# Kernel tuning notes

Measured on AMD Instinct MI355X. Metric: run time of the kernel, lower is better.

Reference implementation:

```python
import jax, jax.numpy as jnp
import numpy as np


def setup_inputs() -> dict:
    key = jax.random.key(0)
    k1, k2, k3, k4 = jax.random.split(key, 4)
    B, S, K, N = 2, 1024, 4096, 4096
    x = jax.random.normal(k1, (B, S, K), dtype=jnp.float32)
    # int8 weights in [-128, 127]
    weight = jax.random.randint(k2, (N, K), -128, 128, dtype=jnp.int8)
    # per-output-channel dequant scales (small positive values)
    scales = jax.random.uniform(k3, (N,), dtype=jnp.float32, minval=0.005, maxval=0.02)
    bias = jax.random.normal(k4, (N,), dtype=jnp.float32) * 0.1
    return {"x": x, "weight": weight, "scales": scales, "bias": bias}


def reference(x, weight, scales, bias):
    # F.linear(x, weight.to(x.dtype)): [B,S,K] @ [N,K]^T -> [B,S,N]
    w = weight.astype(x.dtype)
    y = jnp.einsum('bsk,nk->bsn', x, w)
    # per-output-channel scale + bias epilogue
    return y * scales + bias
```

## Files before the change

kernel.cpp:

```cpp
#include <hip/hip_runtime.h>
#include <hip/hip_bf16.h>
#include <stdint.h>

#define M_DIM 2048
#define N_DIM 4096
#define K_DIM 4096

#define BM 128
#define BN 128
#define BK 128

#define ATILE (BM * BK)
#define BTILE (BN * BK)
#define NT (K_DIM / BK)

typedef __attribute__((ext_vector_type(4))) int   int4v;
typedef __attribute__((ext_vector_type(4))) float f32x4;

__device__ __forceinline__ void load_lds16(const void* g, void* l) {
    __builtin_amdgcn_global_load_lds(
        (const __attribute__((address_space(1))) void*)g,
        (__attribute__((address_space(3))) void*)l,
        16, 0, 0);
}

__global__ __launch_bounds__(256) void quant_x(const float* __restrict__ x,
                                               int8_t* __restrict__ Aq,
                                               float* __restrict__ sx) {
    const int row = blockIdx.x;
    const int tid = threadIdx.x;
    const float4* xr = (const float4*)(x + (size_t)row * K_DIM);

    float4 v[4];
    float mx = 0.f;
#pragma unroll
    for (int p = 0; p < 4; p++) {
        v[p] = xr[p * 256 + tid];
        mx = fmaxf(mx, fmaxf(fmaxf(fabsf(v[p].x), fabsf(v[p].y)),
                             fmaxf(fabsf(v[p].z), fabsf(v[p].w))));
    }
#pragma unroll
    for (int off = 32; off >= 1; off >>= 1)
        mx = fmaxf(mx, __shfl_xor(mx, off, 64));

    __shared__ float wmax[4];
    __shared__ float smax;
    if ((tid & 63) == 0) wmax[tid >> 6] = mx;
    __syncthreads();
    if (tid == 0) {
        float m = fmaxf(fmaxf(wmax[0], wmax[1]), fmaxf(wmax[2], wmax[3]));
        m = fmaxf(m, 1e-20f);
        smax = m;
        sx[row] = m * (1.0f / 127.0f);
    }
    __syncthreads();
    const float inv = 127.0f / smax;

    int* out = (int*)Aq + (size_t)row * (K_DIM / 4);
#pragma unroll
    for (int p = 0; p < 4; p++) {
        int q0 = (int)__builtin_rintf(v[p].x * inv);
        int q1 = (int)__builtin_rintf(v[p].y * inv);
        int q2 = (int)__builtin_rintf(v[p].z * inv);
        int q3 = (int)__builtin_rintf(v[p].w * inv);
        q0 = max(-127, min(127, q0)); q1 = max(-127, min(127, q1));
        q2 = max(-127, min(127, q2)); q3 = max(-127, min(127, q3));
        out[p * 256 + tid] = (q0 & 255) | ((q1 & 255) << 8) |
                             ((q2 & 255) << 16) | ((q3 & 255) << 24);
    }
}

__global__ __launch_bounds__(256) void cvt_w8(const int* __restrict__ w,
                                              int8_t* __restrict__ Bq) {
    size_t i = ((size_t)blockIdx.x * 256 + threadIdx.x) * 16;
    int4 a0 = *(const int4*)(w + i);
    int4 a1 = *(const int4*)(w + i + 4);
    int4 a2 = *(const int4*)(w + i + 8);
    int4 a3 = *(const int4*)(w + i + 12);
    uint4 t;
    t.x = (a0.x & 255) | ((a0.y & 255) << 8) | ((a0.z & 255) << 16) | ((a0.w & 255) << 24);
    t.y = (a1.x & 255) | ((a1.y & 255) << 8) | ((a1.z & 255) << 16) | ((a1.w & 255) << 24);
    t.z = (a2.x & 255) | ((a2.y & 255) << 8) | ((a2.z & 255) << 16) | ((a2.w & 255) << 24);
    t.w = (a3.x & 255) | ((a3.y & 255) << 8) | ((a3.z & 255) << 16) | ((a3.w & 255) << 24);
    *(uint4*)(Bq + i) = t;
}


__global__ __launch_bounds__(512, 4) void gemm_bt_i8(
    const int8_t* __restrict__ A,
    const int8_t* __restrict__ B,
    const float*  __restrict__ sx,
    const float*  __restrict__ scales,
    const float*  __restrict__ bias,
    float* __restrict__ C)
{
    __shared__ __align__(16) int8_t As[2 * ATILE];
    __shared__ __align__(16) int8_t Bs[2 * BTILE];

    const int tid  = threadIdx.x;

    const int bid   = blockIdx.x;
    const int xcd   = bid & 7;
    const int local = bid >> 3;
    const int bm    = (xcd >> 2) * 8 + (local >> 3);
    const int bn    = (xcd & 3) * 8 + (local & 7);

    const int lane = tid & 63;
    const int wave = tid >> 6;
    const int spat = wave & 3;
    const int ks   = wave >> 2;
    const int wm   = (spat >> 1) * 64;
    const int wn   = (spat & 1) * 64;
    const int l16  = lane & 15;
    const int quad = lane >> 4;
    const int swz  = l16 & 7;
    const int cp   = (ks * 4 + quad) ^ swz;

    const int srow = tid >> 3;
    const int cgl  = (tid & 7) ^ (srow & 7);

    const int8_t* ga0 = A + (size_t)(bm * BM + srow)      * K_DIM + cgl * 16;
    const int8_t* ga1 = A + (size_t)(bm * BM + 64 + srow) * K_DIM + cgl * 16;
    const int8_t* gb0 = B + (size_t)(bn * BN + srow)      * K_DIM + cgl * 16;
    const int8_t* gb1 = B + (size_t)(bn * BN + 64 + srow) * K_DIM + cgl * 16;
    const int la0 = tid * 16;
    const int la1 = 8192 + tid * 16;

    load_lds16(ga0, As + la0);
    load_lds16(ga1, As + la1);
    load_lds16(gb0, Bs + la0);
    load_lds16(gb1, Bs + la1);

    int4v acc[4][4] = {};

    int cur = 0;
    for (int k0 = 0; k0 < K_DIM; k0 += BK, cur ^= 1) {
        __syncthreads();

        const int kn = k0 + BK;
        if (kn < K_DIM) {
            const int nb = (cur ^ 1);
            load_lds16(ga0 + kn, As + nb * ATILE + la0);
            load_lds16(ga1 + kn, As + nb * ATILE + la1);
            load_lds16(gb0 + kn, Bs + nb * BTILE + la0);
            load_lds16(gb1 + kn, Bs + nb * BTILE + la1);
        }

        const int8_t* Ab = As + cur * ATILE;
        const int8_t* Bb = Bs + cur * BTILE;

        int4v af[4];
#pragma unroll
        for (int i = 0; i < 4; i++)
            af[i] = *(const int4v*)(Ab + (wm + i * 16 + l16) * BK + cp * 16);
#pragma unroll
        for (int j = 0; j < 4; j++) {
            int4v bf = *(const int4v*)(Bb + (wn + j * 16 + l16) * BK + cp * 16);
#pragma unroll
            for (int i = 0; i < 4; i++)
                acc[i][j] = __builtin_amdgcn_mfma_i32_16x16x64_i8(
                    af[i], bf, acc[i][j], 0, 0, 0);
        }
    }

    __syncthreads();

    int8_t* rbase = (spat < 2 ? As : Bs) + (spat & 1) * 16384;

    if (ks == 1) {
#pragma unroll
        for (int i = 0; i < 4; i++)
#pragma unroll
            for (int j = 0; j < 4; j++)
                *(int4v*)(rbase + ((i * 4 + j) * 64 + lane) * 16) = acc[i][j];
    }
    __syncthreads();

    if (ks == 0) {
#pragma unroll
        for (int i = 0; i < 4; i++)
#pragma unroll
            for (int j = 0; j < 4; j++)
                acc[i][j] += *(const int4v*)(rbase + ((i * 4 + j) * 64 + lane) * 16);

        float sxr[16];
#pragma unroll
        for (int i = 0; i < 4; i++)
#pragma unroll
            for (int r = 0; r < 4; r++)
                sxr[i * 4 + r] = sx[bm * BM + wm + i * 16 + quad * 4 + r];

#pragma unroll
        for (int j = 0; j < 4; j++) {
            const int col = bn * BN + wn + j * 16 + l16;
            const float s = scales[col];
            const float b = bias[col];
#pragma unroll
            for (int i = 0; i < 4; i++) {
                const int row0 = bm * BM + wm + i * 16 + quad * 4;
#pragma unroll
                for (int r = 0; r < 4; r++) {
                    C[(size_t)(row0 + r) * N_DIM + col] =
                        (float)acc[i][j][r] * (sxr[i * 4 + r] * s) + b;
                }
            }
        }
    }
}


extern "C" void kernel_launch(void* const* d_in, const int* in_sizes, int n_in,
                              void* d_out, int out_size, void* d_ws, size_t ws_size,
                              hipStream_t stream) {
    const float* x      = (const float*)d_in[0];
    const int*   w      = (const int*)d_in[1];
    const float* scales = (const float*)d_in[2];
    const float* bias   = (const float*)d_in[3];
    float*       out    = (float*)d_out;

    int8_t* Aq = (int8_t*)d_ws;
    int8_t* Bq = (int8_t*)d_ws + (size_t)M_DIM * K_DIM;
    float*  sx = (float*)((int8_t*)d_ws + (size_t)(M_DIM + N_DIM) * K_DIM);

    quant_x<<<M_DIM, 256, 0, stream>>>(x, Aq, sx);
    cvt_w8<<<(int)((size_t)N_DIM * K_DIM / 16 / 256), 256, 0, stream>>>(w, Bq);

    gemm_bt_i8<<<512, 512, 0, stream>>>(Aq, Bq, sx, scales, bias, out);
}
```

Baseline: 165.0 us.

## Widen GEMM block tile to 128x256 with 1024 threads and 256 blocks

Doubles the N tile to 256 and the block to 16 waves (8 spatial by 2 K-split), launching 256 blocks so each fits one per CU. Each A tile is now reused across twice as many output columns, cutting global and LDS traffic per MFMA. The K-split reduction is done in two LDS passes because the LDS scratch only holds half the partial sums. The risks are one block per CU with no other block to hide barrier stalls, and 256 blocks leaving CUs idle or unevenly loaded.

Result: slower. 168.8 us (+2.3%).

```diff
diff --git a/kernel.cpp b/kernel.cpp
--- a/kernel.cpp
+++ b/kernel.cpp
@@ -7,7 +7,7 @@
 #define K_DIM 4096
 
 #define BM 128
-#define BN 128
+#define BN 256
 #define BK 128
 
 #define ATILE (BM * BK)
@@ -86,7 +86,7 @@
 }
 
 
-__global__ __launch_bounds__(512, 4) void gemm_bt_i8(
+__global__ __launch_bounds__(1024, 1) void gemm_bt_i8(
     const int8_t* __restrict__ A,
     const int8_t* __restrict__ B,
     const float*  __restrict__ sx,
@@ -102,15 +102,15 @@
     const int bid   = blockIdx.x;
     const int xcd   = bid & 7;
     const int local = bid >> 3;
-    const int bm    = (xcd >> 2) * 8 + (local >> 3);
-    const int bn    = (xcd & 3) * 8 + (local & 7);
+    const int bm    = (xcd >> 1) * 4 + (local >> 3);
+    const int bn    = (xcd & 1) * 8 + (local & 7);
 
     const int lane = tid & 63;
     const int wave = tid >> 6;
-    const int spat = wave & 3;
-    const int ks   = wave >> 2;
-    const int wm   = (spat >> 1) * 64;
-    const int wn   = (spat & 1) * 64;
+    const int spat = wave & 7;
+    const int ks   = wave >> 3;
+    const int wm   = (spat >> 2) * 64;
+    const int wn   = (spat & 3) * 64;
     const int l16  = lane & 15;
     const int quad = lane >> 4;
     const int swz  = l16 & 7;
@@ -119,35 +119,29 @@
     const int srow = tid >> 3;
     const int cgl  = (tid & 7) ^ (srow & 7);
 
-    const int8_t* ga0 = A + (size_t)(bm * BM + srow)      * K_DIM + cgl * 16;
-    const int8_t* ga1 = A + (size_t)(bm * BM + 64 + srow) * K_DIM + cgl * 16;
-    const int8_t* gb0 = B + (size_t)(bn * BN + srow)      * K_DIM + cgl * 16;
-    const int8_t* gb1 = B + (size_t)(bn * BN + 64 + srow) * K_DIM + cgl * 16;
-    const int la0 = tid * 16;
-    const int la1 = 8192 + tid * 16;
-
-    load_lds16(ga0, As + la0);
-    load_lds16(ga1, As + la1);
-    load_lds16(gb0, Bs + la0);
-    load_lds16(gb1, Bs + la1);
+    const int8_t* ga  = A + (size_t)(bm * BM + srow)       * K_DIM + cgl * 16;
+    const int8_t* gb0 = B + (size_t)(bn * BN + srow)       * K_DIM + cgl * 16;
+    const int8_t* gb1 = B + (size_t)(bn * BN + 128 + srow) * K_DIM + cgl * 16;
+    const int la = tid * 16;
+
+#define STAGE(slot, k0_) do {                                                \
+        load_lds16(ga  + (k0_), As + (slot) * ATILE + la);                   \
+        load_lds16(gb0 + (k0_), Bs + (slot) * BTILE + la);                   \
+        load_lds16(gb1 + (k0_), Bs + (slot) * BTILE + 16384 + la);           \
+    } while (0)
 
     int4v acc[4][4] = {};
 
-    int cur = 0;
-    for (int k0 = 0; k0 < K_DIM; k0 += BK, cur ^= 1) {
+    STAGE(0, 0);
+
+    for (int t = 0; t < NT; ++t) {
         __syncthreads();
 
-        const int kn = k0 + BK;
-        if (kn < K_DIM) {
-            const int nb = (cur ^ 1);
-            load_lds16(ga0 + kn, As + nb * ATILE + la0);
-            load_lds16(ga1 + kn, As + nb * ATILE + la1);
-            load_lds16(gb0 + kn, Bs + nb * BTILE + la0);
-            load_lds16(gb1 + kn, Bs + nb * BTILE + la1);
-        }
-
-        const int8_t* Ab = As + cur * ATILE;
-        const int8_t* Bb = Bs + cur * BTILE;
+        if (t + 1 < NT)
+            STAGE((t + 1) & 1, (t + 1) * BK);
+
+        const int8_t* Ab = As + (t & 1) * ATILE;
+        const int8_t* Bb = Bs + (t & 1) * BTILE;
 
         int4v af[4];
 #pragma unroll
@@ -163,11 +157,12 @@
         }
     }
 
-    __syncthreads();
-
-    int8_t* rbase = (spat < 2 ? As : Bs) + (spat & 1) * 16384;
-
-    if (ks == 1) {
+#undef STAGE
+
+    int8_t* rbase = ((spat & 3) < 2 ? As : Bs) + (spat & 1) * 16384;
+
+    __syncthreads();
+    if (ks == 1 && spat < 4) {
 #pragma unroll
         for (int i = 0; i < 4; i++)
 #pragma unroll
@@ -175,14 +170,31 @@
                 *(int4v*)(rbase + ((i * 4 + j) * 64 + lane) * 16) = acc[i][j];
     }
     __syncthreads();
+    if (ks == 0 && spat < 4) {
+#pragma unroll
+        for (int i = 0; i < 4; i++)
+#pragma unroll
+            for (int j = 0; j < 4; j++)
+                acc[i][j] += *(const int4v*)(rbase + ((i * 4 + j) * 64 + lane) * 16);
+    }
+    __syncthreads();
+    if (ks == 1 && spat >= 4) {
+#pragma unroll
+        for (int i = 0; i < 4; i++)
+#pragma unroll
+            for (int j = 0; j < 4; j++)
+                *(int4v*)(rbase + ((i * 4 + j) * 64 + lane) * 16) = acc[i][j];
+    }
+    __syncthreads();
+    if (ks == 0 && spat >= 4) {
+#pragma unroll
+        for (int i = 0; i < 4; i++)
+#pragma unroll
+            for (int j = 0; j < 4; j++)
+                acc[i][j] += *(const int4v*)(rbase + ((i * 4 + j) * 64 + lane) * 16);
+    }
 
     if (ks == 0) {
-#pragma unroll
-        for (int i = 0; i < 4; i++)
-#pragma unroll
-            for (int j = 0; j < 4; j++)
-                acc[i][j] += *(const int4v*)(rbase + ((i * 4 + j) * 64 + lane) * 16);
-
         float sxr[16];
 #pragma unroll
         for (int i = 0; i < 4; i++)
@@ -225,5 +237,5 @@
     quant_x<<<M_DIM, 256, 0, stream>>>(x, Aq, sx);
     cvt_w8<<<(int)((size_t)N_DIM * K_DIM / 16 / 256), 256, 0, stream>>>(w, Bq);
 
-    gemm_bt_i8<<<512, 512, 0, stream>>>(Aq, Bq, sx, scales, bias, out);
-}
+    gemm_bt_i8<<<256, 1024, 0, stream>>>(Aq, Bq, sx, scales, bias, out);
+}
```
